# Optimization experiments

Hardware: AMD Instinct MI355X
Metric: run time of the kernel (lower is better)

Reference implementation:

```python
import jax, jax.numpy as jnp
import numpy as np

D_MODEL = 256
N_HEADS = 4
D_FF = 1024
N = 6144
N_DOMS = 1024
LN_EPS = 1e-5
NEG_INF = -1e30


def setup_inputs() -> dict:
    key = jax.random.key(0)
    ks = jax.random.split(key, 10)
    x = jax.random.normal(ks[0], (N, D_MODEL), dtype=jnp.float32)
    pulse_to_dom_idx = jnp.sort(jax.random.randint(ks[1], (N,), 0, N_DOMS, dtype=jnp.int32))
    s = 0.02
    return {
        "x": x,
        "pulse_to_dom_idx": pulse_to_dom_idx,
        "qkv_w": jax.random.normal(ks[2], (D_MODEL, 3 * D_MODEL), dtype=jnp.float32) * s,
        "qkv_b": jnp.zeros((3 * D_MODEL,), dtype=jnp.float32),
        "out_w": jax.random.normal(ks[3], (D_MODEL, D_MODEL), dtype=jnp.float32) * s,
        "out_b": jnp.zeros((D_MODEL,), dtype=jnp.float32),
        "ff_w1": jax.random.normal(ks[4], (D_MODEL, D_FF), dtype=jnp.float32) * s,
        "ff_b1": jnp.zeros((D_FF,), dtype=jnp.float32),
        "ff_w2": jax.random.normal(ks[5], (D_FF, D_MODEL), dtype=jnp.float32) * s,
        "ff_b2": jnp.zeros((D_MODEL,), dtype=jnp.float32),
        "ln1_g": jnp.ones((D_MODEL,), dtype=jnp.float32),
        "ln1_b": jnp.zeros((D_MODEL,), dtype=jnp.float32),
        "ln2_g": jnp.ones((D_MODEL,), dtype=jnp.float32),
        "ln2_b": jnp.zeros((D_MODEL,), dtype=jnp.float32),
    }


def _layer_norm(x, g, b):
    mu = jnp.mean(x, axis=-1, keepdims=True)
    var = jnp.mean(jnp.square(x - mu), axis=-1, keepdims=True)
    return (x - mu) * jax.lax.rsqrt(var + LN_EPS) * g + b


def reference(x, pulse_to_dom_idx, qkv_w, qkv_b, out_w, out_b,
              ff_w1, ff_b1, ff_w2, ff_b2, ln1_g, ln1_b, ln2_g, ln2_b):
    n, d = x.shape
    hd = d // N_HEADS
    # --- document-masked multi-head attention (dense, matching FlexAttention score_mod) ---
    qkv = x @ qkv_w + qkv_b                      # (N, 3D)
    q, k, v = jnp.split(qkv, 3, axis=-1)
    q = q.reshape(n, N_HEADS, hd)
    k = k.reshape(n, N_HEADS, hd)
    v = v.reshape(n, N_HEADS, hd)
    scores = jnp.einsum('qhd,khd->hqk', q, k) / jnp.sqrt(jnp.float32(hd))  # (H, N, N)
    same_doc = pulse_to_dom_idx[:, None] == pulse_to_dom_idx[None, :]      # (N, N)
    scores = jnp.where(same_doc[None], scores, NEG_INF)
    attn = jax.nn.softmax(scores, axis=-1)
    attn_out = jnp.einsum('hqk,khd->qhd', attn, v).reshape(n, d)
    attn_out = attn_out @ out_w + out_b
    # --- residual + norm + FFN + residual + norm (dropout in eval mode) ---
    x = _layer_norm(x + attn_out, ln1_g, ln1_b)
    ff = jax.nn.gelu(x @ ff_w1 + ff_b1, approximate=False) @ ff_w2 + ff_b2
    x = _layer_norm(x + ff, ln2_g, ln2_b)
    return x
```

## Files before the change

kernel.cpp:

```cpp
#include <hip/hip_runtime.h>
#include <hip/hip_bf16.h>
#include <math.h>

constexpr int NP  = 6144;
constexpr int DM  = 256;
constexpr int DFF = 1024;
constexpr float LNEPS = 1e-5f;

typedef __attribute__((ext_vector_type(8))) short short8;
typedef __attribute__((ext_vector_type(4))) short short4v;
typedef __attribute__((ext_vector_type(4))) float f32x4;

__device__ __forceinline__ short f2bf(float f) {
    unsigned u = __builtin_bit_cast(unsigned, f);
    unsigned r = u + 0x7FFFu + ((u >> 16) & 1u);
    return (short)(r >> 16);
}
__device__ __forceinline__ float bf2f(short s) {
    unsigned u = ((unsigned)(unsigned short)s) << 16;
    return __builtin_bit_cast(float, u);
}

#define GLOAD16(gp, lp)                                                        \
    __builtin_amdgcn_global_load_lds(                                          \
        (const __attribute__((address_space(1))) unsigned int*)(gp),           \
        (__attribute__((address_space(3))) unsigned int*)(lp), 16, 0, 0)

__device__ __forceinline__ int lds_idx(int row, int chunk) {
    return row * 64 + ((chunk ^ (row & 7)) * 8);
}
__device__ __forceinline__ int lds_idx128(int row, int chunk) {
    return row * 128 + ((chunk ^ (row & 7)) * 8);
}

__global__ __launch_bounds__(256) void prep_kernel(
    const float* __restrict__ qkv_w, const float* __restrict__ out_w,
    const float* __restrict__ ff_w1, const float* __restrict__ ff_w2,
    short* __restrict__ qkvT, short* __restrict__ outT,
    short* __restrict__ ff1T, short* __restrict__ ff2T,
    const int* __restrict__ dom, int* __restrict__ seg_s,
    int* __restrict__ seg_e, const float* __restrict__ x,
    short* __restrict__ xB) {
    int b = blockIdx.x;
    if (b >= 792) {
        int i = (b - 792) * 2048 + threadIdx.x * 8;
        float4 a0 = *(const float4*)&x[i];
        float4 a1 = *(const float4*)&x[i + 4];
        short8 v = { f2bf(a0.x), f2bf(a0.y), f2bf(a0.z), f2bf(a0.w),
                     f2bf(a1.x), f2bf(a1.y), f2bf(a1.z), f2bf(a1.w) };
        *(short8*)&xB[i] = v;
        return;
    }
    if (b >= 768) {
        int i = (b - 768) * 256 + threadIdx.x;
        if (i >= NP) return;
        int d = dom[i];
        int s = i;
        while (s > 0 && dom[s - 1] == d) --s;
        int e = i + 1;
        while (e < NP && dom[e] == d) ++e;
        seg_s[i] = s;
        seg_e[i] = e;
        return;
    }
    const float* src;
    short* dst;
    int K, Nn;
    if (b < 192)      { src = qkv_w; dst = qkvT; K = 256;  Nn = 768; }
    else if (b < 256) { b -= 192; src = out_w; dst = outT; K = 256;  Nn = 256; }
    else if (b < 512) { b -= 256; src = ff_w1; dst = ff1T; K = 256;  Nn = 1024; }
    else              { b -= 512; src = ff_w2; dst = ff2T; K = 1024; Nn = 256; }
    int tpr = Nn / 32;
    int k0 = (b / tpr) * 32, n0 = (b % tpr) * 32;

    __shared__ float lds[32][36];
    int t = threadIdx.x;
    {
        int k = t >> 3, n = (t & 7) * 4;
        *(float4*)&lds[k][n] = *(const float4*)&src[(size_t)(k0 + k) * Nn + n0 + n];
    }
    __syncthreads();
    {
        int n = t >> 3, ks = (t & 7) * 4;
        short4v o = { f2bf(lds[ks + 0][n]), f2bf(lds[ks + 1][n]),
                      f2bf(lds[ks + 2][n]), f2bf(lds[ks + 3][n]) };
        *(short4v*)&dst[(size_t)(n0 + n) * K + k0 + ks] = o;
    }
}

template <int EPI>
__global__ __launch_bounds__(256) void mgemm128x64(
    const short* __restrict__ A, const short* __restrict__ Bt,
    const float* __restrict__ bias, short* __restrict__ C, int Nn, int K) {
    __shared__ __align__(16) short As[128 * 128];
    __shared__ __align__(16) short Bs[64 * 128];

    const int tid = threadIdx.x, lane = tid & 63, w = tid >> 6;
    const int wm = (w >> 1) * 64, wn = (w & 1) * 32;

    const int nx = gridDim.x;
    const int bid = blockIdx.y * nx + blockIdx.x;
    const int q = (nx * gridDim.y) >> 3;
    const int id2 = (bid & 7) * q + (bid >> 3);
    const int rowBase = (id2 / nx) * 128, colBase = (id2 % nx) * 64;

    const int lr4 = lane >> 4;
    const int c16 = lane & 15;
    const int fr = lane & 15, g4 = lane >> 4;

    f32x4 acc[4][2];
#pragma unroll
    for (int i = 0; i < 4; ++i)
#pragma unroll
        for (int j = 0; j < 2; ++j) acc[i][j] = f32x4{0.f, 0.f, 0.f, 0.f};

    for (int k0 = 0; k0 < K; k0 += 128) {
#pragma unroll
        for (int i = 0; i < 12; ++i) {
            int g = w * 12 + i;
            if (g < 32) {
                int row = g * 4 + lr4;
                int sc = c16 ^ (row & 7);
                GLOAD16(A + (size_t)(rowBase + row) * K + k0 + sc * 8, &As[g * 512]);
            } else {
                int row = (g - 32) * 4 + lr4;
                int sc = c16 ^ (row & 7);
                GLOAD16(Bt + (size_t)(colBase + row) * K + k0 + sc * 8,
                        &Bs[(g - 32) * 512]);
            }
        }
        __syncthreads();

#pragma unroll
        for (int kk = 0; kk < 4; ++kk) {
            int j = kk * 4 + g4;
            short8 af[4], bfv[2];
#pragma unroll
            for (int f = 0; f < 4; ++f)
                af[f] = *(const short8*)&As[lds_idx128(wm + f * 16 + fr, j)];
#pragma unroll
            for (int f = 0; f < 2; ++f)
                bfv[f] = *(const short8*)&Bs[lds_idx128(wn + f * 16 + fr, j)];
#pragma unroll
            for (int fm = 0; fm < 4; ++fm)
#pragma unroll
                for (int fn = 0; fn < 2; ++fn)
                    acc[fm][fn] = __builtin_amdgcn_mfma_f32_16x16x32_bf16(
                        af[fm], bfv[fn], acc[fm][fn], 0, 0, 0);
        }
        __syncthreads();
    }

    const int cr = g4 * 4;
#pragma unroll
    for (int fm = 0; fm < 4; ++fm)
#pragma unroll
        for (int fn = 0; fn < 2; ++fn) {
            int c = colBase + wn + fn * 16 + fr;
            float bv = bias[c];
#pragma unroll
            for (int j = 0; j < 4; ++j) {
                int r = rowBase + wm + fm * 16 + cr + j;
                float v = acc[fm][fn][j] + bv;
                if (EPI == 1) v = 0.5f * v * (1.0f + erff(v * 0.70710678118654752f));
                C[(size_t)r * Nn + c] = f2bf(v);
            }
        }
}

__global__ __launch_bounds__(512) void gemmln16(
    const short* __restrict__ A, const short* __restrict__ Bt,
    const float* __restrict__ bias, const short* __restrict__ res,
    const float* __restrict__ gw, const float* __restrict__ bw,
    float* __restrict__ out) {
    __shared__ __align__(16) short As[16 * 128];
    __shared__ __align__(16) short Bs[256 * 128];
    __shared__ float r1[8][16], r2[8][16];

    const int tid = threadIdx.x, lane = tid & 63, w = tid >> 6;
    const int rowBase = blockIdx.x * 16;
    const int lr4 = lane >> 4, c16 = lane & 15;
    const int fr = lane & 15, g4 = lane >> 4;

    f32x4 acc[2];
    acc[0] = f32x4{0.f, 0.f, 0.f, 0.f};
    acc[1] = f32x4{0.f, 0.f, 0.f, 0.f};

    for (int k0 = 0; k0 < 1024; k0 += 128) {
        if (w < 4) {
            int row = w * 4 + lr4;
            int sc = c16 ^ (row & 7);
            GLOAD16(A + (size_t)(rowBase + row) * 1024 + k0 + sc * 8, &As[w * 512]);
        }
#pragma unroll
        for (int i = 0; i < 8; ++i) {
            int g = w * 8 + i;
            int row = g * 4 + lr4;
            int sc = c16 ^ (row & 7);
            GLOAD16(Bt + (size_t)row * 1024 + k0 + sc * 8, &Bs[g * 512]);
        }
        __syncthreads();
#pragma unroll
        for (int kk = 0; kk < 4; ++kk) {
            int j = kk * 4 + g4;
            short8 af = *(const short8*)&As[lds_idx128(fr, j)];
            short8 bfv[2];
#pragma unroll
            for (int fn = 0; fn < 2; ++fn)
                bfv[fn] = *(const short8*)&Bs[lds_idx128(w * 32 + fn * 16 + fr, j)];
#pragma unroll
            for (int fn = 0; fn < 2; ++fn)
                acc[fn] = __builtin_amdgcn_mfma_f32_16x16x32_bf16(
                    af, bfv[fn], acc[fn], 0, 0, 0);
        }
        __syncthreads();
    }

    float v[2][4], p1[4], p2[4];
#pragma unroll
    for (int j = 0; j < 4; ++j) { p1[j] = 0.f; p2[j] = 0.f; }
#pragma unroll
    for (int fn = 0; fn < 2; ++fn) {
        int c = w * 32 + fn * 16 + fr;
        float bv = bias[c];
#pragma unroll
        for (int j = 0; j < 4; ++j) {
            int r = rowBase + g4 * 4 + j;
            float t = acc[fn][j] + bv + bf2f(res[(size_t)r * 256 + c]);
            v[fn][j] = t;
            p1[j] += t;
            p2[j] += t * t;
        }
    }
#pragma unroll
    for (int m = 1; m < 16; m <<= 1)
#pragma unroll
        for (int j = 0; j < 4; ++j) {
            p1[j] += __shfl_xor(p1[j], m);
            p2[j] += __shfl_xor(p2[j], m);
        }
    if (fr == 0) {
#pragma unroll
        for (int j = 0; j < 4; ++j) {
            r1[w][g4 * 4 + j] = p1[j];
            r2[w][g4 * 4 + j] = p2[j];
        }
    }
    __syncthreads();
#pragma unroll
    for (int j = 0; j < 4; ++j) {
        int rl = g4 * 4 + j;
        int r = rowBase + rl;
        float s1 = 0.f, s2 = 0.f;
#pragma unroll
        for (int ww = 0; ww < 8; ++ww) { s1 += r1[ww][rl]; s2 += r2[ww][rl]; }
        float mu = s1 * (1.0f / 256.0f);
        float var = s2 * (1.0f / 256.0f) - mu * mu;
        float rstd = rsqrtf(var + LNEPS);
#pragma unroll
        for (int fn = 0; fn < 2; ++fn) {
            int c = w * 32 + fn * 16 + fr;
            out[(size_t)r * 256 + c] = (v[fn][j] - mu) * rstd * gw[c] + bw[c];
        }
    }
}

__global__ __launch_bounds__(512) void attnln_kernel(
    const short* __restrict__ qkvB, const int* __restrict__ seg_s,
    const int* __restrict__ seg_e, const short* __restrict__ outT,
    const float* __restrict__ out_b, const float* __restrict__ xres,
    const float* __restrict__ gw, const float* __restrict__ bw,
    short* __restrict__ x1) {
    __shared__ __align__(16) short As[16 * 256];
    __shared__ __align__(16) short Bs[256 * 128];
    __shared__ float r1[8][16], r2[8][16];

    const int tid = threadIdx.x, lane = tid & 63, w = tid >> 6;
    const int rowBase = blockIdx.x * 16;
    const int lr4 = lane >> 4, c16 = lane & 15;
    const int fr = lane & 15, g4 = lane >> 4;

    {
        const int l8 = lane & 7;
        const int G  = (w << 3) | (lane >> 3);
        int r = G >> 2, h = G & 3;
        int row = rowBase + r;
        short8 qv = *(const short8*)&qkvB[(size_t)row * 768 + h * 64 + l8 * 8];
        float qd[8];
#pragma unroll
        for (int e = 0; e < 8; ++e) qd[e] = bf2f(qv[e]);
        int ss = seg_s[row], ee = seg_e[row];
        float m = -INFINITY, l = 0.0f;
        float acc[8] = {0.f, 0.f, 0.f, 0.f, 0.f, 0.f, 0.f, 0.f};
        for (int j = ss; j < ee; ++j) {
            short8 kv = *(const short8*)&qkvB[(size_t)j * 768 + 256 + h * 64 + l8 * 8];
            short8 vv = *(const short8*)&qkvB[(size_t)j * 768 + 512 + h * 64 + l8 * 8];
            float prod = 0.f;
#pragma unroll
            for (int e = 0; e < 8; ++e) prod += qd[e] * bf2f(kv[e]);
            prod += __shfl_xor(prod, 1);
            prod += __shfl_xor(prod, 2);
            prod += __shfl_xor(prod, 4);
            float score = prod * 0.125f;
            float mn = fmaxf(m, score);
            float scale = __expf(m - mn);
            float p = __expf(score - mn);
            l = l * scale + p;
#pragma unroll
            for (int e = 0; e < 8; ++e) acc[e] = acc[e] * scale + p * bf2f(vv[e]);
            m = mn;
        }
        float inv = 1.0f / l;
        int c = h * 8 + l8;
        short8 o;
#pragma unroll
        for (int e = 0; e < 8; ++e) o[e] = f2bf(acc[e] * inv);
        *(short8*)&As[r * 256 + ((c ^ (r & 7)) * 8)] = o;
    }
    __syncthreads();

    f32x4 acc[2];
    acc[0] = f32x4{0.f, 0.f, 0.f, 0.f};
    acc[1] = f32x4{0.f, 0.f, 0.f, 0.f};

    for (int k0 = 0; k0 < 256; k0 += 128) {
#pragma unroll
        for (int i = 0; i < 8; ++i) {
            int g = w * 8 + i;
            int row = g * 4 + lr4;
            int sc = c16 ^ (row & 7);
            GLOAD16(outT + (size_t)row * 256 + k0 + sc * 8, &Bs[g * 512]);
        }
        __syncthreads();
        __builtin_amdgcn_s_setprio(1);
#pragma unroll
        for (int kk = 0; kk < 4; ++kk) {
            int j = kk * 4 + g4;
            int cj = (k0 >> 3) + j;
            short8 af = *(const short8*)&As[fr * 256 + ((cj ^ (fr & 7)) * 8)];
            short8 bfv[2];
#pragma unroll
            for (int fn = 0; fn < 2; ++fn)
                bfv[fn] = *(const short8*)&Bs[lds_idx128(w * 32 + fn * 16 + fr, j)];
#pragma unroll
            for (int fn = 0; fn < 2; ++fn)
                acc[fn] = __builtin_amdgcn_mfma_f32_16x16x32_bf16(
                    af, bfv[fn], acc[fn], 0, 0, 0);
        }
        __builtin_amdgcn_s_setprio(0);
        __syncthreads();
    }

    float v[2][4], p1[4], p2[4];
#pragma unroll
    for (int j = 0; j < 4; ++j) { p1[j] = 0.f; p2[j] = 0.f; }
#pragma unroll
    for (int fn = 0; fn < 2; ++fn) {
        int c = w * 32 + fn * 16 + fr;
        float bv = out_b[c];
#pragma unroll
        for (int j = 0; j < 4; ++j) {
            int r = rowBase + g4 * 4 + j;
            float t = acc[fn][j] + bv + xres[(size_t)r * 256 + c];
            v[fn][j] = t;
            p1[j] += t;
            p2[j] += t * t;
        }
    }
#pragma unroll
    for (int m = 1; m < 16; m <<= 1)
#pragma unroll
        for (int j = 0; j < 4; ++j) {
            p1[j] += __shfl_xor(p1[j], m);
            p2[j] += __shfl_xor(p2[j], m);
        }
    if (fr == 0) {
#pragma unroll
        for (int j = 0; j < 4; ++j) {
            r1[w][g4 * 4 + j] = p1[j];
            r2[w][g4 * 4 + j] = p2[j];
        }
    }
    __syncthreads();
#pragma unroll
    for (int j = 0; j < 4; ++j) {
        int rl = g4 * 4 + j;
        int r = rowBase + rl;
        float s1 = 0.f, s2 = 0.f;
#pragma unroll
        for (int ww = 0; ww < 8; ++ww) { s1 += r1[ww][rl]; s2 += r2[ww][rl]; }
        float mu = s1 * (1.0f / 256.0f);
        float var = s2 * (1.0f / 256.0f) - mu * mu;
        float rstd = rsqrtf(var + LNEPS);
#pragma unroll
        for (int fn = 0; fn < 2; ++fn) {
            int c = w * 32 + fn * 16 + fr;
            float o = (v[fn][j] - mu) * rstd * gw[c] + bw[c];
            x1[(size_t)r * 256 + c] = f2bf(o);
        }
    }
}

extern "C" void kernel_launch(void* const* d_in, const int* in_sizes, int n_in,
                              void* d_out, int out_size, void* d_ws, size_t ws_size,
                              hipStream_t stream) {
    const float* x      = (const float*)d_in[0];
    const int*   dom    = (const int*)d_in[1];
    const float* qkv_w  = (const float*)d_in[2];
    const float* qkv_b  = (const float*)d_in[3];
    const float* out_w  = (const float*)d_in[4];
    const float* out_b  = (const float*)d_in[5];
    const float* ff_w1  = (const float*)d_in[6];
    const float* ff_b1  = (const float*)d_in[7];
    const float* ff_w2  = (const float*)d_in[8];
    const float* ff_b2  = (const float*)d_in[9];
    const float* ln1_g  = (const float*)d_in[10];
    const float* ln1_b  = (const float*)d_in[11];
    const float* ln2_g  = (const float*)d_in[12];
    const float* ln2_b  = (const float*)d_in[13];
    float* out = (float*)d_out;

    short* xB     = (short*)d_ws;
    short* qkvB   = xB + (size_t)NP * 256;
    short* x1     = qkvB + (size_t)NP * 768;
    short* hB     = x1 + (size_t)NP * 256;
    short* qkvT   = hB + (size_t)NP * 1024;
    short* outT   = qkvT + 768 * 256;
    short* ff1T   = outT + 256 * 256;
    short* ff2T   = ff1T + 1024 * 256;
    int* seg_s    = (int*)(ff2T + 256 * 1024);
    int* seg_e    = seg_s + NP;

    prep_kernel<<<1560, 256, 0, stream>>>(qkv_w, out_w, ff_w1, ff_w2,
                                          qkvT, outT, ff1T, ff2T,
                                          dom, seg_s, seg_e, x, xB);

    mgemm128x64<0><<<dim3(768 / 64, NP / 128), 256, 0, stream>>>(
        xB, qkvT, qkv_b, qkvB, 768, 256);

    attnln_kernel<<<NP / 16, 512, 0, stream>>>(
        qkvB, seg_s, seg_e, outT, out_b, x, ln1_g, ln1_b, x1);

    mgemm128x64<1><<<dim3(DFF / 64, NP / 128), 256, 0, stream>>>(
        x1, ff1T, ff_b1, hB, 1024, 256);

    gemmln16<<<NP / 16, 512, 0, stream>>>(
        hB, ff2T, ff_b2, x1, ln2_g, ln2_b, out);
}
```

Measured before the change: 61.95 us.

## Widen FFN2+LN tile to 32 rows, remap block ids, read bf16 residual

The final FFN2+LayerNorm kernel now handles 32 rows per block instead of 16. This halves the number of times the 256x1024 weight tile is reloaded, and every wave now takes part in loading A. Both fused LN kernels remap block indices in an interleaved (bid&7) pattern so that neighbouring blocks land differently, which is likely aimed at XCD/L2 locality. The attention kernel now reads the residual as bf16 from the converted copy of x instead of fp32, which halves that traffic but loses precision in the residual. The setprio hints are also removed.

```diff
diff --git a/kernel.cpp b/kernel.cpp
--- a/kernel.cpp
+++ b/kernel.cpp
@@ -168,26 +168,31 @@
         }
 }
 
-__global__ __launch_bounds__(512) void gemmln16(
+__global__ __launch_bounds__(512) void gemmln32(
     const short* __restrict__ A, const short* __restrict__ Bt,
     const float* __restrict__ bias, const short* __restrict__ res,
     const float* __restrict__ gw, const float* __restrict__ bw,
     float* __restrict__ out) {
-    __shared__ __align__(16) short As[16 * 128];
+    __shared__ __align__(16) short As[32 * 128];
     __shared__ __align__(16) short Bs[256 * 128];
-    __shared__ float r1[8][16], r2[8][16];
+    __shared__ float r1[8][32], r2[8][32];
 
     const int tid = threadIdx.x, lane = tid & 63, w = tid >> 6;
-    const int rowBase = blockIdx.x * 16;
+    const int bid = blockIdx.x;
+    const int q = gridDim.x >> 3;
+    const int id2 = (bid & 7) * q + (bid >> 3);
+    const int rowBase = id2 * 32;
     const int lr4 = lane >> 4, c16 = lane & 15;
     const int fr = lane & 15, g4 = lane >> 4;
 
-    f32x4 acc[2];
-    acc[0] = f32x4{0.f, 0.f, 0.f, 0.f};
-    acc[1] = f32x4{0.f, 0.f, 0.f, 0.f};
+    f32x4 acc[2][2];
+#pragma unroll
+    for (int i = 0; i < 2; ++i)
+#pragma unroll
+        for (int j = 0; j < 2; ++j) acc[i][j] = f32x4{0.f, 0.f, 0.f, 0.f};
 
     for (int k0 = 0; k0 < 1024; k0 += 128) {
-        if (w < 4) {
+        {
             int row = w * 4 + lr4;
             int sc = c16 ^ (row & 7);
             GLOAD16(A + (size_t)(rowBase + row) * 1024 + k0 + sc * 8, &As[w * 512]);
@@ -203,72 +208,86 @@
 #pragma unroll
         for (int kk = 0; kk < 4; ++kk) {
             int j = kk * 4 + g4;
-            short8 af = *(const short8*)&As[lds_idx128(fr, j)];
-            short8 bfv[2];
+            short8 af[2], bfv[2];
+#pragma unroll
+            for (int fm = 0; fm < 2; ++fm)
+                af[fm] = *(const short8*)&As[lds_idx128(fm * 16 + fr, j)];
 #pragma unroll
             for (int fn = 0; fn < 2; ++fn)
                 bfv[fn] = *(const short8*)&Bs[lds_idx128(w * 32 + fn * 16 + fr, j)];
 #pragma unroll
-            for (int fn = 0; fn < 2; ++fn)
-                acc[fn] = __builtin_amdgcn_mfma_f32_16x16x32_bf16(
-                    af, bfv[fn], acc[fn], 0, 0, 0);
-        }
-        __syncthreads();
-    }
-
-    float v[2][4], p1[4], p2[4];
-#pragma unroll
-    for (int j = 0; j < 4; ++j) { p1[j] = 0.f; p2[j] = 0.f; }
-#pragma unroll
-    for (int fn = 0; fn < 2; ++fn) {
-        int c = w * 32 + fn * 16 + fr;
-        float bv = bias[c];
-#pragma unroll
-        for (int j = 0; j < 4; ++j) {
-            int r = rowBase + g4 * 4 + j;
-            float t = acc[fn][j] + bv + bf2f(res[(size_t)r * 256 + c]);
-            v[fn][j] = t;
-            p1[j] += t;
-            p2[j] += t * t;
-        }
-    }
-#pragma unroll
-    for (int m = 1; m < 16; m <<= 1)
-#pragma unroll
-        for (int j = 0; j < 4; ++j) {
-            p1[j] += __shfl_xor(p1[j], m);
-            p2[j] += __shfl_xor(p2[j], m);
-        }
-    if (fr == 0) {
-#pragma unroll
-        for (int j = 0; j < 4; ++j) {
-            r1[w][g4 * 4 + j] = p1[j];
-            r2[w][g4 * 4 + j] = p2[j];
-        }
-    }
-    __syncthreads();
-#pragma unroll
-    for (int j = 0; j < 4; ++j) {
-        int rl = g4 * 4 + j;
-        int r = rowBase + rl;
-        float s1 = 0.f, s2 = 0.f;
-#pragma unroll
-        for (int ww = 0; ww < 8; ++ww) { s1 += r1[ww][rl]; s2 += r2[ww][rl]; }
-        float mu = s1 * (1.0f / 256.0f);
-        float var = s2 * (1.0f / 256.0f) - mu * mu;
-        float rstd = rsqrtf(var + LNEPS);
+            for (int fm = 0; fm < 2; ++fm)
+#pragma unroll
+                for (int fn = 0; fn < 2; ++fn)
+                    acc[fm][fn] = __builtin_amdgcn_mfma_f32_16x16x32_bf16(
+                        af[fm], bfv[fn], acc[fm][fn], 0, 0, 0);
+        }
+        __syncthreads();
+    }
+
+    float v[2][2][4], p1[2][4], p2[2][4];
+#pragma unroll
+    for (int fm = 0; fm < 2; ++fm)
+#pragma unroll
+        for (int j = 0; j < 4; ++j) { p1[fm][j] = 0.f; p2[fm][j] = 0.f; }
+#pragma unroll
+    for (int fm = 0; fm < 2; ++fm)
 #pragma unroll
         for (int fn = 0; fn < 2; ++fn) {
             int c = w * 32 + fn * 16 + fr;
-            out[(size_t)r * 256 + c] = (v[fn][j] - mu) * rstd * gw[c] + bw[c];
-        }
-    }
+            float bv = bias[c];
+#pragma unroll
+            for (int j = 0; j < 4; ++j) {
+                int r = rowBase + fm * 16 + g4 * 4 + j;
+                float t = acc[fm][fn][j] + bv + bf2f(res[(size_t)r * 256 + c]);
+                v[fm][fn][j] = t;
+                p1[fm][j] += t;
+                p2[fm][j] += t * t;
+            }
+        }
+#pragma unroll
+    for (int m = 1; m < 16; m <<= 1)
+#pragma unroll
+        for (int fm = 0; fm < 2; ++fm)
+#pragma unroll
+            for (int j = 0; j < 4; ++j) {
+                p1[fm][j] += __shfl_xor(p1[fm][j], m);
+                p2[fm][j] += __shfl_xor(p2[fm][j], m);
+            }
+    if (fr == 0) {
+#pragma unroll
+        for (int fm = 0; fm < 2; ++fm)
+#pragma unroll
+            for (int j = 0; j < 4; ++j) {
+                r1[w][fm * 16 + g4 * 4 + j] = p1[fm][j];
+                r2[w][fm * 16 + g4 * 4 + j] = p2[fm][j];
+            }
+    }
+    __syncthreads();
+#pragma unroll
+    for (int fm = 0; fm < 2; ++fm)
+#pragma unroll
+        for (int j = 0; j < 4; ++j) {
+            int rl = fm * 16 + g4 * 4 + j;
+            int r = rowBase + rl;
+            float s1 = 0.f, s2 = 0.f;
+#pragma unroll
+            for (int ww = 0; ww < 8; ++ww) { s1 += r1[ww][rl]; s2 += r2[ww][rl]; }
+            float mu = s1 * (1.0f / 256.0f);
+            float var = s2 * (1.0f / 256.0f) - mu * mu;
+            float rstd = rsqrtf(var + LNEPS);
+#pragma unroll
+            for (int fn = 0; fn < 2; ++fn) {
+                int c = w * 32 + fn * 16 + fr;
+                out[(size_t)r * 256 + c] = (v[fm][fn][j] - mu) * rstd * gw[c] + bw[c];
+            }
+        }
 }
 
 __global__ __launch_bounds__(512) void attnln_kernel(
     const short* __restrict__ qkvB, const int* __restrict__ seg_s,
     const int* __restrict__ seg_e, const short* __restrict__ outT,
-    const float* __restrict__ out_b, const float* __restrict__ xres,
+    const float* __restrict__ out_b, const short* __restrict__ xres,
     const float* __restrict__ gw, const float* __restrict__ bw,
     short* __restrict__ x1) {
     __shared__ __align__(16) short As[16 * 256];
@@ -276,7 +295,10 @@
     __shared__ float r1[8][16], r2[8][16];
 
     const int tid = threadIdx.x, lane = tid & 63, w = tid >> 6;
-    const int rowBase = blockIdx.x * 16;
+    const int bid = blockIdx.x;
+    const int q = gridDim.x >> 3;
+    const int id2 = (bid & 7) * q + (bid >> 3);
+    const int rowBase = id2 * 16;
     const int lr4 = lane >> 4, c16 = lane & 15;
     const int fr = lane & 15, g4 = lane >> 4;
 
@@ -332,7 +354,6 @@
             GLOAD16(outT + (size_t)row * 256 + k0 + sc * 8, &Bs[g * 512]);
         }
         __syncthreads();
-        __builtin_amdgcn_s_setprio(1);
 #pragma unroll
         for (int kk = 0; kk < 4; ++kk) {
             int j = kk * 4 + g4;
@@ -347,7 +368,6 @@
                 acc[fn] = __builtin_amdgcn_mfma_f32_16x16x32_bf16(
                     af, bfv[fn], acc[fn], 0, 0, 0);
         }
-        __builtin_amdgcn_s_setprio(0);
         __syncthreads();
     }
 
@@ -361,7 +381,7 @@
 #pragma unroll
         for (int j = 0; j < 4; ++j) {
             int r = rowBase + g4 * 4 + j;
-            float t = acc[fn][j] + bv + xres[(size_t)r * 256 + c];
+            float t = acc[fn][j] + bv + bf2f(xres[(size_t)r * 256 + c]);
             v[fn][j] = t;
             p1[j] += t;
             p2[j] += t * t;
@@ -439,11 +459,11 @@
         xB, qkvT, qkv_b, qkvB, 768, 256);
 
     attnln_kernel<<<NP / 16, 512, 0, stream>>>(
-        qkvB, seg_s, seg_e, outT, out_b, x, ln1_g, ln1_b, x1);
+        qkvB, seg_s, seg_e, outT, out_b, xB, ln1_g, ln1_b, x1);
 
     mgemm128x64<1><<<dim3(DFF / 64, NP / 128), 256, 0, stream>>>(
         x1, ff1T, ff_b1, hB, 1024, 256);
 
-    gemmln16<<<NP / 16, 512, 0, stream>>>(
+    gemmln32<<<NP / 32, 512, 0, stream>>>(
         hB, ff2T, ff_b2, x1, ln2_g, ln2_b, out);
 }
```

Result: no change. 62.53 us (+0.9%).
